# Performance work log

Hardware: AMD Instinct MI355X
Metric: run time of the kernel (lower is better)

The kernel has to match this reference:

```python
import jax, jax.numpy as jnp
import numpy as np

N_BITS = 14
L = 1 << N_BITS
B, C_IN, C_OUT = 32, 32, 64

def _neigh_idx():
    # (L, n_bits): index j flipped at bit b -> j ^ (1<<b)
    s = jnp.arange(L)
    return jnp.stack([s ^ (1 << b) for b in range(N_BITS)], axis=1)

def setup_inputs() -> dict:
    key = jax.random.key(0)
    k1, k2, k3, k4 = jax.random.split(key, 4)
    x = jax.random.normal(k1, (B, C_IN, L), dtype=jnp.float32)
    w_self = jnp.ones((), dtype=jnp.float32)
    w_bits = jax.random.normal(k2, (N_BITS,), dtype=jnp.float32) * 0.1
    # Conv1d(kernel_size=1) weight squeezed to (C_out, C_in)
    mix_w = jax.random.normal(k3, (C_OUT, C_IN), dtype=jnp.float32) * (1.0 / np.sqrt(C_IN))
    mix_b = jax.random.normal(k4, (C_OUT,), dtype=jnp.float32) * 0.01
    return {"x": x, "w_self": w_self, "w_bits": w_bits, "mix_w": mix_w, "mix_b": mix_b}

def reference(x, w_self, w_bits, mix_w, mix_b):
    n_bits = w_bits.shape[0]
    idx = _neigh_idx()                          # (L, n_bits), int32
    xn = x[:, :, idx]                           # (B, C, L, n_bits) XOR-neighbor gather
    neigh_sum = jnp.einsum('bclk,k->bcl', xn, w_bits)
    y = w_self * x + neigh_sum
    y = y / (1.0 + n_bits)                      # agg == 'mean'
    # 1x1 conv mix: (B,C,L) x (C_out,C_in) -> (B,C_out,L)
    return jnp.einsum('bcl,oc->bol', y, mix_w) + mix_b[None, :, None]
```

## Files before the change

kernel.cpp:

```cpp
#include <hip/hip_runtime.h>

#define TILE  256
#define CIN   32
#define COUT  64
#define LSIZE 16384
#define NBITS 14

typedef float vfloat4 __attribute__((ext_vector_type(4)));

__global__ __launch_bounds__(256, 4)
void hamming_fused(const float* __restrict__ x,
                   const float* __restrict__ w_self,
                   const float* __restrict__ w_bits,
                   const float* __restrict__ mix_w,
                   const float* __restrict__ mix_b,
                   float* __restrict__ out)
{
    __shared__ float xs[CIN][TILE];
    __shared__ float mws[CIN][COUT];

    const int tid = threadIdx.x;

    const int d    = blockIdx.x;
    const int xcd  = d & 7;
    const int j    = d >> 3;
    const int b    = xcd * 4 + (j >> 6);
    const int tile = j & 63;
    const int base = tile * TILE;
    const float* xb = x + (size_t)b * CIN * LSIZE;

    #pragma unroll
    for (int i = 0; i < (CIN * COUT) / 256; ++i) {
        int g = tid + i * 256;
        int o = g >> 5, c = g & 31;
        mws[c][o] = mix_w[g];
    }

    #pragma unroll
    for (int i = 0; i < (CIN * TILE) / (256 * 4); ++i) {
        int idx = tid + i * 256;
        int r  = idx >> 6;
        int c4 = (idx & 63) << 2;
        *(float4*)&xs[r][c4] =
            *(const float4*)(xb + (size_t)r * LSIZE + base + c4);
    }
    __syncthreads();

    const float ws = w_self[0];
    float wb[NBITS];
    #pragma unroll
    for (int k = 0; k < NBITS; ++k) wb[k] = w_bits[k];

    const int t    = tid;
    const int gcol = base + t;
    float yreg[CIN];

    #pragma unroll
    for (int c0 = 0; c0 < CIN; c0 += 8) {
        float pf[8][6];
        #pragma unroll
        for (int cc = 0; cc < 8; ++cc) {
            const float* xr = xb + (size_t)(c0 + cc) * LSIZE;
            #pragma unroll
            for (int k = 0; k < 6; ++k)
                pf[cc][k] = xr[gcol ^ (TILE << k)];
        }
        #pragma unroll
        for (int cc = 0; cc < 8; ++cc) {
            int c = c0 + cc;
            float a = ws * xs[c][t];
            #pragma unroll
            for (int k = 0; k < 8; ++k)
                a += wb[k] * xs[c][t ^ (1 << k)];
            #pragma unroll
            for (int k = 0; k < 6; ++k)
                a += wb[8 + k] * pf[cc][k];
            yreg[c] = a * (1.0f / 15.0f);
        }
    }
    __syncthreads();

    #pragma unroll
    for (int c = 0; c < CIN; ++c) xs[c][t] = yreg[c];
    __syncthreads();

    const int tx   = tid & 63;
    const int ty   = tid >> 6;
    const int colb = tx << 2;
    const int o0   = ty * 16;

    float4 acc[16];
    #pragma unroll
    for (int jj = 0; jj < 16; ++jj) {
        float bias = mix_b[o0 + jj];
        acc[jj] = make_float4(bias, bias, bias, bias);
    }

    #pragma unroll 4
    for (int c = 0; c < CIN; ++c) {
        float4 yv = *(float4*)&xs[c][colb];
        #pragma unroll
        for (int j4 = 0; j4 < 4; ++j4) {
            float4 m = *(float4*)&mws[c][o0 + j4 * 4];
            acc[j4*4+0].x += m.x * yv.x; acc[j4*4+0].y += m.x * yv.y;
            acc[j4*4+0].z += m.x * yv.z; acc[j4*4+0].w += m.x * yv.w;
            acc[j4*4+1].x += m.y * yv.x; acc[j4*4+1].y += m.y * yv.y;
            acc[j4*4+1].z += m.y * yv.z; acc[j4*4+1].w += m.y * yv.w;
            acc[j4*4+2].x += m.z * yv.x; acc[j4*4+2].y += m.z * yv.y;
            acc[j4*4+2].z += m.z * yv.z; acc[j4*4+2].w += m.z * yv.w;
            acc[j4*4+3].x += m.w * yv.x; acc[j4*4+3].y += m.w * yv.y;
            acc[j4*4+3].z += m.w * yv.z; acc[j4*4+3].w += m.w * yv.w;
        }
    }

    float* ob = out + (size_t)b * COUT * LSIZE;
    #pragma unroll
    for (int jj = 0; jj < 16; ++jj) {
        vfloat4 v; v.x = acc[jj].x; v.y = acc[jj].y; v.z = acc[jj].z; v.w = acc[jj].w;
        vfloat4* p = (vfloat4*)(ob + (size_t)(o0 + jj) * LSIZE + base + colb);
        __builtin_nontemporal_store(v, p);
    }
}

extern "C" void kernel_launch(void* const* d_in, const int* in_sizes, int n_in,
                              void* d_out, int out_size, void* d_ws, size_t ws_size,
                              hipStream_t stream) {
    const float* x      = (const float*)d_in[0];
    const float* w_self = (const float*)d_in[1];
    const float* w_bits = (const float*)d_in[2];
    const float* mix_w  = (const float*)d_in[3];
    const float* mix_b  = (const float*)d_in[4];
    float* out = (float*)d_out;

    hamming_fused<<<dim3(2048), 256, 0, stream>>>(x, w_self, w_bits, mix_w, mix_b, out);
}
```

Measured before the change: 209.5 us.

## Load x tile directly into LDS and vectorize neighbor aggregation by float4

Replaces the register-staged float4 tile copy with direct global-to-LDS loads (global_load_lds). The aggregation is remapped so each wave handles 8 channels and each lane 4 consecutive columns. Bit-0/1 neighbors come from in-register swizzles, and high-bit neighbors are fetched as float4 global loads instead of scalar gathers. The aim is fewer load instructions and less LDS traffic, at the cost of a different thread-to-data mapping and more vector registers.

```diff
diff --git a/kernel.cpp b/kernel.cpp
--- a/kernel.cpp
+++ b/kernel.cpp
@@ -6,6 +6,7 @@
 #define LSIZE 16384
 #define NBITS 14
 
+typedef float f32x4   __attribute__((ext_vector_type(4)));
 typedef float vfloat4 __attribute__((ext_vector_type(4)));
 
 __global__ __launch_bounds__(256, 4)
@@ -19,7 +20,9 @@
     __shared__ float xs[CIN][TILE];
     __shared__ float mws[CIN][COUT];
 
-    const int tid = threadIdx.x;
+    const int tid  = threadIdx.x;
+    const int lane = tid & 63;
+    const int wv   = tid >> 6;
 
     const int d    = blockIdx.x;
     const int xcd  = d & 7;
@@ -37,57 +40,65 @@
     }
 
     #pragma unroll
-    for (int i = 0; i < (CIN * TILE) / (256 * 4); ++i) {
-        int idx = tid + i * 256;
-        int r  = idx >> 6;
-        int c4 = (idx & 63) << 2;
-        *(float4*)&xs[r][c4] =
-            *(const float4*)(xb + (size_t)r * LSIZE + base + c4);
+    for (int i = 0; i < 8; ++i) {
+        const int r = wv + i * 4;
+        const float* src = xb + (size_t)r * LSIZE + base + lane * 4;
+        __builtin_amdgcn_global_load_lds(
+            (const __attribute__((address_space(1))) void*)src,
+            (__attribute__((address_space(3))) void*)&xs[r][lane * 4],
+            16, 0, 0);
     }
-    __syncthreads();
 
     const float ws = w_self[0];
     float wb[NBITS];
     #pragma unroll
     for (int k = 0; k < NBITS; ++k) wb[k] = w_bits[k];
 
-    const int t    = tid;
-    const int gcol = base + t;
-    float yreg[CIN];
+    __syncthreads();
 
+    const int c0   = wv * 8;
+    const int colb = lane * 4;
+
+    f32x4 yv[8];
     #pragma unroll
-    for (int c0 = 0; c0 < CIN; c0 += 8) {
-        float pf[8][6];
+    for (int cc = 0; cc < 8; cc += 2) {
+        f32x4 pf[2][6];
         #pragma unroll
-        for (int cc = 0; cc < 8; ++cc) {
-            const float* xr = xb + (size_t)(c0 + cc) * LSIZE;
+        for (int u = 0; u < 2; ++u) {
+            const float* xr = xb + (size_t)(c0 + cc + u) * LSIZE;
             #pragma unroll
-            for (int k = 0; k < 6; ++k)
-                pf[cc][k] = xr[gcol ^ (TILE << k)];
+            for (int kk = 0; kk < 6; ++kk)
+                pf[u][kk] = *(const f32x4*)(xr + ((base ^ (TILE << kk)) + colb));
         }
         #pragma unroll
-        for (int cc = 0; cc < 8; ++cc) {
-            int c = c0 + cc;
-            float a = ws * xs[c][t];
+        for (int u = 0; u < 2; ++u) {
+            const int c = c0 + cc + u;
+            const f32x4 s = *(const f32x4*)&xs[c][colb];
+            f32x4 a = s * ws;
+            a.x += wb[0] * s.y; a.y += wb[0] * s.x; a.z += wb[0] * s.w; a.w += wb[0] * s.z;
+            a.x += wb[1] * s.z; a.y += wb[1] * s.w; a.z += wb[1] * s.x; a.w += wb[1] * s.y;
             #pragma unroll
-            for (int k = 0; k < 8; ++k)
-                a += wb[k] * xs[c][t ^ (1 << k)];
+            for (int k = 2; k < 8; ++k) {
+                const f32x4 t = *(const f32x4*)&xs[c][colb ^ (1 << k)];
+                a += wb[k] * t;
+            }
             #pragma unroll
-            for (int k = 0; k < 6; ++k)
-                a += wb[8 + k] * pf[cc][k];
-            yreg[c] = a * (1.0f / 15.0f);
+            for (int kk = 0; kk < 6; ++kk)
+                a += wb[8 + kk] * pf[u][kk];
+            yv[cc + u] = a * (1.0f / 15.0f);
         }
     }
     __syncthreads();
 
     #pragma unroll
-    for (int c = 0; c < CIN; ++c) xs[c][t] = yreg[c];
+    for (int cc = 0; cc < 8; ++cc)
+        *(f32x4*)&xs[c0 + cc][colb] = yv[cc];
     __syncthreads();
 
-    const int tx   = tid & 63;
-    const int ty   = tid >> 6;
-    const int colb = tx << 2;
-    const int o0   = ty * 16;
+    const int tx  = tid & 63;
+    const int ty  = tid >> 6;
+    const int cb2 = tx << 2;
+    const int o0  = ty * 16;
 
     float4 acc[16];
     #pragma unroll
@@ -98,18 +109,18 @@
 
     #pragma unroll 4
     for (int c = 0; c < CIN; ++c) {
-        float4 yv = *(float4*)&xs[c][colb];
+        float4 yc = *(float4*)&xs[c][cb2];
         #pragma unroll
         for (int j4 = 0; j4 < 4; ++j4) {
             float4 m = *(float4*)&mws[c][o0 + j4 * 4];
-            acc[j4*4+0].x += m.x * yv.x; acc[j4*4+0].y += m.x * yv.y;
-            acc[j4*4+0].z += m.x * yv.z; acc[j4*4+0].w += m.x * yv.w;
-            acc[j4*4+1].x += m.y * yv.x; acc[j4*4+1].y += m.y * yv.y;
-            acc[j4*4+1].z += m.y * yv.z; acc[j4*4+1].w += m.y * yv.w;
-            acc[j4*4+2].x += m.z * yv.x; acc[j4*4+2].y += m.z * yv.y;
-            acc[j4*4+2].z += m.z * yv.z; acc[j4*4+2].w += m.z * yv.w;
-            acc[j4*4+3].x += m.w * yv.x; acc[j4*4+3].y += m.w * yv.y;
-            acc[j4*4+3].z += m.w * yv.z; acc[j4*4+3].w += m.w * yv.w;
+            acc[j4*4+0].x += m.x * yc.x; acc[j4*4+0].y += m.x * yc.y;
+            acc[j4*4+0].z += m.x * yc.z; acc[j4*4+0].w += m.x * yc.w;
+            acc[j4*4+1].x += m.y * yc.x; acc[j4*4+1].y += m.y * yc.y;
+            acc[j4*4+1].z += m.y * yc.z; acc[j4*4+1].w += m.y * yc.w;
+            acc[j4*4+2].x += m.z * yc.x; acc[j4*4+2].y += m.z * yc.y;
+            acc[j4*4+2].z += m.z * yc.z; acc[j4*4+2].w += m.z * yc.w;
+            acc[j4*4+3].x += m.w * yc.x; acc[j4*4+3].y += m.w * yc.y;
+            acc[j4*4+3].z += m.w * yc.z; acc[j4*4+3].w += m.w * yc.w;
         }
     }
 
@@ -117,7 +128,7 @@
     #pragma unroll
     for (int jj = 0; jj < 16; ++jj) {
         vfloat4 v; v.x = acc[jj].x; v.y = acc[jj].y; v.z = acc[jj].z; v.w = acc[jj].w;
-        vfloat4* p = (vfloat4*)(ob + (size_t)(o0 + jj) * LSIZE + base + colb);
+        vfloat4* p = (vfloat4*)(ob + (size_t)(o0 + jj) * LSIZE + base + cb2);
         __builtin_nontemporal_store(v, p);
     }
 }
```

After: 219.1 us. +4.6%, slower.
